# Optimization experiments

Measured on AMD Instinct MI355X. Metric: run time of the kernel, lower is better.

The kernel has to match this reference:

```python
import jax, jax.numpy as jnp
from jax import lax
import numpy as np

SIGMAS = (30.0, 150.0, 300.0)
RESTORE_FACTOR = 2.0
COLOR_GAIN = 10.0
GAIN = 270.0
OFFSET = 128.0
EPS = 1e-6


def _dwconv(x, k2d, stride):
    # depthwise 2D conv, NCHW, VALID padding (caller pads)
    C = x.shape[1]
    kh, kw = k2d.shape
    w = jnp.broadcast_to(k2d.astype(x.dtype)[None, None], (C, 1, kh, kw))
    return lax.conv_general_dilated(
        x, w, (stride, stride), 'VALID',
        dimension_numbers=('NCHW', 'OIHW', 'NCHW'),
        feature_group_count=C)


def _pyr_down(x):
    # cv2.pyrDown: 5x5 binomial kernel, reflect-101 border, stride-2 decimation
    k1 = jnp.array([1., 4., 6., 4., 1.], jnp.float32) / 16.0
    k2 = jnp.outer(k1, k1)
    xp = jnp.pad(x, ((0, 0), (0, 0), (2, 2), (2, 2)), mode='reflect')
    return _dwconv(xp, k2, 2)


def _gauss_blur(x, ksize):
    # cv2.GaussianBlur with sigmaX=0: sigma derived from kernel size
    s = 0.3 * ((ksize - 1) * 0.5 - 1.0) + 0.8
    i = jnp.arange(ksize, dtype=jnp.float32) - (ksize - 1) / 2.0
    g = jnp.exp(-(i * i) / (2.0 * s * s))
    g = g / g.sum()
    k2 = jnp.outer(g, g)
    p = ksize // 2
    xp = jnp.pad(x, ((0, 0), (0, 0), (p, p), (p, p)), mode='reflect')
    return _dwconv(xp, k2, 1)


def _fast_filter(x, sigma):
    # Faithful port of GaussianBlurConv.FastFilter (static Python recursion:
    # sigma is a compile-time constant, so depth is fixed at trace time).
    sigma = min(sigma, 300.0)
    k = int(round(sigma * 3 * 2 + 1)) | 1
    if k < 3:
        return x
    if k < 10:
        return _gauss_blur(x, k)
    h, w = x.shape[2], x.shape[3]
    if h < 2 or w < 2:
        return x
    sub = _fast_filter(_pyr_down(x), sigma / 2.0)
    # cv2.resize default INTER_LINEAR == half-pixel bilinear
    return jax.image.resize(sub, (x.shape[0], x.shape[1], h, w), method='bilinear')


def _msr_forward(x):
    img = x * 255.0 + 1.0                      # (N,3,H,W)
    log_img = jnp.log10(img + EPS)
    retinex = sum(log_img - jnp.log10(_fast_filter(img, s) + EPS) for s in SIGMAS)
    retinex = retinex / len(SIGMAS)
    img_sum = jnp.sum(img, axis=1, keepdims=True)   # (N,1,H,W)
    color_rest = jnp.log10(img * RESTORE_FACTOR / (img_sum + EPS) + 1.0)
    enhanced = retinex * color_rest * COLOR_GAIN * GAIN + OFFSET
    return jnp.clip(enhanced, 0.0, 255.0) / 255.0


def setup_inputs() -> dict:
    key = jax.random.key(0)
    x = jax.random.uniform(key, (8, 3, 1280, 1280), dtype=jnp.float32)
    return {"x": x}


def reference(x):
    return _msr_forward(x)
```

## Files before the change

kernel.cpp:

```cpp
#include <hip/hip_runtime.h>

#define NC 24

typedef float f32x4 __attribute__((ext_vector_type(4)));

__device__ __forceinline__ float pyr_point(const float* ip, int Hi, int Wi, int oy, int ox)
{
    const float k1[5] = {0.0625f, 0.25f, 0.375f, 0.25f, 0.0625f};
    float acc = 0.f;
#pragma unroll
    for (int i = 0; i < 5; ++i) {
        int y = 2 * oy - 2 + i;
        y = (y < 0) ? -y : y;
        y = (y >= Hi) ? (2 * Hi - 2 - y) : y;
        const float* rp = ip + (size_t)y * Wi;
        float r = 0.f;
#pragma unroll
        for (int j = 0; j < 5; ++j) {
            int xx = 2 * ox - 2 + j;
            xx = (xx < 0) ? -xx : xx;
            xx = (xx >= Wi) ? (2 * Wi - 2 - xx) : xx;
            r = fmaf(k1[j], rp[xx], r);
        }
        acc = fmaf(k1[i], r, acc);
    }
    return acc;
}

template <int K>
__device__ __forceinline__ float blur_point(const float* ip, int H, int W, int oy, int ox,
                                            const float* w)
{
    const int R = K / 2;
    float acc = 0.f;
#pragma unroll
    for (int i = 0; i < K; ++i) {
        int y = oy - R + i;
        y = (y < 0) ? -y : y;
        y = (y >= H) ? (2 * H - 2 - y) : y;
        const float* rp = ip + (size_t)y * W;
        float r = 0.f;
#pragma unroll
        for (int j = 0; j < K; ++j) {
            int xx = ox - R + j;
            xx = (xx < 0) ? -xx : xx;
            xx = (xx >= W) ? (2 * W - 2 - xx) : xx;
            r = fmaf(w[j], rp[xx], r);
        }
        acc = fmaf(w[i], r, acc);
    }
    return acc;
}

__global__ void __launch_bounds__(256) pyrdown4_kernel(
    const float* __restrict__ in, float* __restrict__ out,
    int Hi, int Wi, int Ho, int Wo, float scale, float offs)
{
    int qx = blockIdx.x * blockDim.x + threadIdx.x;
    int oy = blockIdx.y * blockDim.y + threadIdx.y;
    int nc = blockIdx.z;
    int ox0 = qx * 4;
    if (ox0 >= Wo || oy >= Ho) return;
    const float* ip = in + (size_t)nc * Hi * Wi;
    const float k[5] = {0.0625f, 0.25f, 0.375f, 0.25f, 0.0625f};

    bool fastx = (qx >= 1) && (8 * qx + 11 <= Wi - 1) && (ox0 + 3 < Wo);
    bool fasty = (oy >= 1) && (2 * oy + 2 <= Hi - 1);
    if (fastx && fasty) {
        int x0 = 8 * qx - 4;
        float col[11];
#pragma unroll
        for (int j = 0; j < 11; ++j) col[j] = 0.f;
        const float* rp = ip + (size_t)(2 * oy - 2) * Wi + x0;
#pragma unroll
        for (int i = 0; i < 5; ++i) {
            f32x4 a = *(const f32x4*)(rp);
            f32x4 b = *(const f32x4*)(rp + 4);
            f32x4 c4 = *(const f32x4*)(rp + 8);
            f32x4 d = *(const f32x4*)(rp + 12);
            float rv[16] = {a[0], a[1], a[2], a[3], b[0], b[1], b[2], b[3],
                            c4[0], c4[1], c4[2], c4[3], d[0], d[1], d[2], d[3]};
#pragma unroll
            for (int j = 0; j < 11; ++j) col[j] = fmaf(k[i], rv[j + 2], col[j]);
            rp += Wi;
        }
        f32x4 o;
#pragma unroll
        for (int p = 0; p < 4; ++p) {
            float s = 0.f;
#pragma unroll
            for (int j = 0; j < 5; ++j) s = fmaf(k[j], col[2 * p + j], s);
            o[p] = fmaf(s, scale, offs);
        }
        *(f32x4*)&out[((size_t)nc * Ho + oy) * Wo + ox0] = o;
    } else {
#pragma unroll
        for (int p = 0; p < 4; ++p) {
            int ox = ox0 + p;
            if (ox < Wo)
                out[((size_t)nc * Ho + oy) * Wo + ox] =
                    fmaf(pyr_point(ip, Hi, Wi, oy, ox), scale, offs);
        }
    }
}

__global__ void __launch_bounds__(256) base_kernel(
    const float* __restrict__ L4g, float* __restrict__ b30g,
    float* __restrict__ b150g, float* __restrict__ b300g)
{
    __shared__ float sL4[80 * 80];
    __shared__ float sL5[40 * 40];
    __shared__ float sL6[20 * 20];
    __shared__ float sL7[10 * 10];
    __shared__ float sL8[5 * 5];
    const int nc = blockIdx.x;
    const int tid = threadIdx.x;

    float w7[7], w9[9];
    {
        float s = 1.4f, s2 = 2.f * s * s, sum = 0.f;
#pragma unroll
        for (int i = 0; i < 7; ++i) { float d = (float)i - 3.f; w7[i] = expf(-(d * d) / s2); sum += w7[i]; }
#pragma unroll
        for (int i = 0; i < 7; ++i) w7[i] /= sum;
        s = 1.7f; s2 = 2.f * s * s; sum = 0.f;
#pragma unroll
        for (int i = 0; i < 9; ++i) { float d = (float)i - 4.f; w9[i] = expf(-(d * d) / s2); sum += w9[i]; }
#pragma unroll
        for (int i = 0; i < 9; ++i) w9[i] /= sum;
    }

    const float* src = L4g + (size_t)nc * 6400;
    for (int i = tid; i < 1600; i += 256)
        *(f32x4*)&sL4[4 * i] = *(const f32x4*)&src[4 * i];
    __syncthreads();
    for (int i = tid; i < 1600; i += 256) {
        int oy = i / 40, ox = i - oy * 40;
        sL5[i] = pyr_point(sL4, 80, 80, oy, ox);
    }
    __syncthreads();
    for (int i = tid; i < 400; i += 256) {
        int oy = i / 20, ox = i - oy * 20;
        sL6[i] = pyr_point(sL5, 40, 40, oy, ox);
    }
    __syncthreads();
    for (int i = tid; i < 100; i += 256) {
        int oy = i / 10, ox = i - oy * 10;
        sL7[i] = pyr_point(sL6, 20, 20, oy, ox);
    }
    __syncthreads();
    for (int i = tid; i < 25; i += 256) {
        int oy = i / 5, ox = i - oy * 5;
        sL8[i] = pyr_point(sL7, 10, 10, oy, ox);
    }
    __syncthreads();
    for (int i = tid; i < 1600; i += 256) {
        int oy = i / 40, ox = i - oy * 40;
        b30g[(size_t)nc * 1600 + i] = blur_point<7>(sL5, 40, 40, oy, ox, w7);
    }
    for (int i = tid; i < 100; i += 256) {
        int oy = i / 10, ox = i - oy * 10;
        b150g[(size_t)nc * 100 + i] = blur_point<9>(sL7, 10, 10, oy, ox, w9);
    }
    for (int i = tid; i < 25; i += 256) {
        int oy = i / 5, ox = i - oy * 5;
        b300g[(size_t)nc * 25 + i] = blur_point<9>(sL8, 5, 5, oy, ox, w9);
    }
}

__global__ void __launch_bounds__(256) mega_final(
    const float* __restrict__ x,
    const float* __restrict__ b30g,
    const float* __restrict__ b150g,
    const float* __restrict__ b300g,
    float* __restrict__ out)
{
    const int H = 1280, W = 1280;
    __shared__ float S[3 * 1963];

    const int tid = threadIdx.x;
    const int X0 = blockIdx.x * 64, Y0 = blockIdx.y * 64;
    const int n = blockIdx.z;

    const int LS[7] = {320, 160, 80, 40, 20, 10, 5};
    int ay[7], by[7], ax[7], bx[7];
    ay[0] = max(0, Y0 / 4 - 1); by[0] = min(319, Y0 / 4 + 16);
    ax[0] = max(0, X0 / 4 - 1); bx[0] = min(319, X0 / 4 + 16);
#pragma unroll
    for (int l = 1; l < 7; ++l) {
        ay[l] = max(0, (ay[l - 1] >> 1) - 1); by[l] = min(LS[l] - 1, (by[l - 1] >> 1) + 1);
        ax[l] = max(0, (ax[l - 1] >> 1) - 1); bx[l] = min(LS[l] - 1, (bx[l - 1] >> 1) + 1);
    }
    const int o300t[7] = {1639, 1495, 1414, 1365, 1329, 1293, 1268};
    const int o150t[6] = {944, 800, 719, 670, 634, 598};
    const int o30t[4]  = {274, 130, 49, 0};

    {
        int ny = by[3] - ay[3] + 1, nx = bx[3] - ax[3] + 1;
        for (int i = tid; i < 3 * ny * nx; i += 256) {
            int c = i / (ny * nx), pt = i - c * (ny * nx);
            int ry = pt / nx, rx = pt - ry * nx;
            S[c * 1963 + o30t[3] + pt] =
                b30g[(size_t)(n * 3 + c) * 1600 + (ay[3] + ry) * 40 + ax[3] + rx];
        }
        ny = by[5] - ay[5] + 1; nx = bx[5] - ax[5] + 1;
        for (int i = tid; i < 3 * ny * nx; i += 256) {
            int c = i / (ny * nx), pt = i - c * (ny * nx);
            int ry = pt / nx, rx = pt - ry * nx;
            S[c * 1963 + o150t[5] + pt] =
                b150g[(size_t)(n * 3 + c) * 100 + (ay[5] + ry) * 10 + ax[5] + rx];
        }
        ny = by[6] - ay[6] + 1; nx = bx[6] - ax[6] + 1;
        for (int i = tid; i < 3 * ny * nx; i += 256) {
            int c = i / (ny * nx), pt = i - c * (ny * nx);
            int ry = pt / nx, rx = pt - ry * nx;
            S[c * 1963 + o300t[6] + pt] =
                b300g[(size_t)(n * 3 + c) * 25 + (ay[6] + ry) * 5 + ax[6] + rx];
        }
    }
    __syncthreads();

#pragma unroll
    for (int l = 5; l >= 0; --l) {
        int srcO[9], dstO[9];
        int m = 0;
#pragma unroll
        for (int c = 0; c < 3; ++c) { srcO[m] = c * 1963 + o300t[l + 1]; dstO[m] = c * 1963 + o300t[l]; ++m; }
        if (l <= 4) {
#pragma unroll
            for (int c = 0; c < 3; ++c) { srcO[m] = c * 1963 + o150t[l + 1]; dstO[m] = c * 1963 + o150t[l]; ++m; }
        }
        if (l <= 2) {
#pragma unroll
            for (int c = 0; c < 3; ++c) { srcO[m] = c * 1963 + o30t[l + 1]; dstO[m] = c * 1963 + o30t[l]; ++m; }
        }
        int ny = by[l] - ay[l] + 1, nx = bx[l] - ax[l] + 1;
        int nxS = bx[l + 1] - ax[l + 1] + 1;
        int Ssrc = LS[l + 1];
        int npts = ny * nx;
        for (int i = tid; i < m * npts; i += 256) {
            int p = i / npts, pt = i - p * npts;
            int ry = pt / nx, rx = pt - ry * nx;
            int oy = ay[l] + ry, ox = ax[l] + rx;
            int my = oy >> 1, py = oy & 1;
            int mx = ox >> 1, px = ox & 1;
            int yA = py ? my : max(my - 1, 0);
            int yB = py ? min(my + 1, Ssrc - 1) : my;
            float wyA = py ? 0.75f : 0.25f, wyB = py ? 0.25f : 0.75f;
            int xA = px ? mx : max(mx - 1, 0);
            int xB = px ? min(mx + 1, Ssrc - 1) : mx;
            float wxA = px ? 0.75f : 0.25f, wxB = px ? 0.25f : 0.75f;
            const float* sp = &S[srcO[p]];
            int la = (yA - ay[l + 1]) * nxS - ax[l + 1];
            int lb = (yB - ay[l + 1]) * nxS - ax[l + 1];
            float v = wyA * (wxA * sp[la + xA] + wxB * sp[la + xB]) +
                      wyB * (wxA * sp[lb + xA] + wxB * sp[lb + xB]);
            S[dstO[p] + pt] = v;
        }
        __syncthreads();
    }

    int tyi = tid >> 4, txi = tid & 15;
    int byi = Y0 / 4 + tyi, bxi = X0 / 4 + txi;
    int nx0 = bx[0] - ax[0] + 1;
    int ry[3], rx[3];
    ry[0] = (byi > 0 ? byi - 1 : 0) - ay[0]; ry[1] = byi - ay[0];
    ry[2] = (byi < 319 ? byi + 1 : 319) - ay[0];
    rx[0] = (bxi > 0 ? bxi - 1 : 0) - ax[0]; rx[1] = bxi - ax[0];
    rx[2] = (bxi < 319 ? bxi + 1 : 319) - ax[0];
    const float WP[4][3] = {{0.375f, 0.625f, 0.f},
                            {0.1875f, 0.75f, 0.0625f},
                            {0.0625f, 0.75f, 0.1875f},
                            {0.f, 0.625f, 0.375f}};
    const int ol0[3] = {274, 944, 1639};

    f32x4 xi[3][4];
#pragma unroll
    for (int c = 0; c < 3; ++c)
#pragma unroll
        for (int qy = 0; qy < 4; ++qy)
            xi[c][qy] = __builtin_nontemporal_load(
                (const f32x4*)&x[((size_t)(n * 3 + c) * H + 4 * byi + qy) * W + 4 * bxi]);

    float crcp[4][4];
#pragma unroll
    for (int qy = 0; qy < 4; ++qy)
#pragma unroll
        for (int qx = 0; qx < 4; ++qx) {
            float s = (xi[0][qy][qx] + xi[1][qy][qx] + xi[2][qy][qx]) * 255.f + 3.f;
            crcp[qy][qx] = __fdividef(2.f, s + 1e-6f);
        }

#pragma unroll
    for (int c = 0; c < 3; ++c) {
        float prod[4][4];
#pragma unroll
        for (int qy = 0; qy < 4; ++qy)
#pragma unroll
            for (int qx = 0; qx < 4; ++qx) prod[qy][qx] = 1.f;

#pragma unroll
        for (int s = 0; s < 3; ++s) {
            const float* fp = &S[c * 1963 + ol0[s]];
            float v[3][3];
#pragma unroll
            for (int i = 0; i < 3; ++i)
#pragma unroll
                for (int j = 0; j < 3; ++j) v[i][j] = fp[ry[i] * nx0 + rx[j]];
#pragma unroll
            for (int qy = 0; qy < 4; ++qy) {
                float vy0 = WP[qy][0] * v[0][0] + WP[qy][1] * v[1][0] + WP[qy][2] * v[2][0];
                float vy1 = WP[qy][0] * v[0][1] + WP[qy][1] * v[1][1] + WP[qy][2] * v[2][1];
                float vy2 = WP[qy][0] * v[0][2] + WP[qy][1] * v[1][2] + WP[qy][2] * v[2][2];
#pragma unroll
                for (int qx = 0; qx < 4; ++qx) {
                    float val = WP[qx][0] * vy0 + WP[qx][1] * vy1 + WP[qx][2] * vy2;
                    prod[qy][qx] *= (val + 1e-6f);
                }
            }
        }

#pragma unroll
        for (int qy = 0; qy < 4; ++qy) {
            f32x4 o;
#pragma unroll
            for (int qx = 0; qx < 4; ++qx) {
                float img = xi[c][qy][qx] * 255.f + 1.f;
                float a = img + 1e-6f;
                float l2a = __log2f(__fdividef(a * a * a, prod[qy][qx]));
                float carg = fmaf(img, crcp[qy][qx], 1.f);
                float l2c = __log2f(carg);
                float e = fmaf(l2a * l2c, 81.55715246f, 128.f);
                e = fminf(fmaxf(e, 0.f), 255.f);
                o[qx] = e * (1.f / 255.f);
            }
            __builtin_nontemporal_store(
                o, (f32x4*)&out[((size_t)(n * 3 + c) * H + 4 * byi + qy) * W + 4 * bxi]);
        }
    }
}

extern "C" void kernel_launch(void* const* d_in, const int* in_sizes, int n_in,
                              void* d_out, int out_size, void* d_ws, size_t ws_size,
                              hipStream_t stream)
{
    const float* x = (const float*)d_in[0];
    float* out = (float*)d_out;
    float* ws = (float*)d_ws;

    size_t off = 0;
    auto alloc = [&](int d) { float* p = ws + off; off += (size_t)NC * d * d; return p; };
    float* L1 = alloc(640);
    float* L2 = alloc(320);
    float* L3 = alloc(160);
    float* L4 = alloc(80);
    float* b30 = alloc(40);
    float* b150 = alloc(10);
    float* b300 = alloc(5);
    (void)ws_size; (void)in_sizes; (void)n_in; (void)out_size;

    dim3 blk(32, 8, 1);
    auto grid4 = [&](int Wo, int Ho) { return dim3((Wo / 4 + 31) / 32, (Ho + 7) / 8, NC); };

    pyrdown4_kernel<<<grid4(640, 640), blk, 0, stream>>>(x,  L1, 1280, 1280, 640, 640, 255.f, 1.f);
    pyrdown4_kernel<<<grid4(320, 320), blk, 0, stream>>>(L1, L2, 640, 640, 320, 320, 1.f, 0.f);
    pyrdown4_kernel<<<grid4(160, 160), blk, 0, stream>>>(L2, L3, 320, 320, 160, 160, 1.f, 0.f);
    pyrdown4_kernel<<<grid4(80,  80),  blk, 0, stream>>>(L3, L4, 160, 160, 80, 80, 1.f, 0.f);
    base_kernel<<<dim3(NC, 1, 1), dim3(256, 1, 1), 0, stream>>>(L4, b30, b150, b300);
    mega_final<<<dim3(20, 20, 8), dim3(256, 1, 1), 0, stream>>>(x, b30, b150, b300, out);
}
```

Measured before the change: 424.7 us.

## Rewrite pyrDown as separable two-pass LDS-tiled kernel; factor bilinear upsample

```diff
diff --git a/kernel.cpp b/kernel.cpp
--- a/kernel.cpp
+++ b/kernel.cpp
@@ -52,55 +52,49 @@
     return acc;
 }
 
-__global__ void __launch_bounds__(256) pyrdown4_kernel(
+__global__ void __launch_bounds__(256) pyrdown_lds_kernel(
     const float* __restrict__ in, float* __restrict__ out,
     int Hi, int Wi, int Ho, int Wo, float scale, float offs)
 {
-    int qx = blockIdx.x * blockDim.x + threadIdx.x;
-    int oy = blockIdx.y * blockDim.y + threadIdx.y;
-    int nc = blockIdx.z;
-    int ox0 = qx * 4;
-    if (ox0 >= Wo || oy >= Ho) return;
+    const int TW = 132;
+    __shared__ float vs[16 * TW];
+    const int tid = threadIdx.x;
+    const int OX = blockIdx.x * 64;
+    const int OY = blockIdx.y * 16;
+    const int nc = blockIdx.z;
+    const float k1[5] = {0.0625f, 0.25f, 0.375f, 0.25f, 0.0625f};
     const float* ip = in + (size_t)nc * Hi * Wi;
-    const float k[5] = {0.0625f, 0.25f, 0.375f, 0.25f, 0.0625f};
-
-    bool fastx = (qx >= 1) && (8 * qx + 11 <= Wi - 1) && (ox0 + 3 < Wo);
-    bool fasty = (oy >= 1) && (2 * oy + 2 <= Hi - 1);
-    if (fastx && fasty) {
-        int x0 = 8 * qx - 4;
-        float col[11];
-#pragma unroll
-        for (int j = 0; j < 11; ++j) col[j] = 0.f;
-        const float* rp = ip + (size_t)(2 * oy - 2) * Wi + x0;
+
+    for (int idx = tid; idx < 16 * TW; idx += 256) {
+        int r = idx / TW;
+        int c = idx - r * TW;
+        int oy = OY + r;
+        if (oy >= Ho) oy = Ho - 1;
+        int xc = 2 * OX - 2 + c;
+        xc = (xc < 0) ? -xc : xc;
+        xc = (xc >= Wi) ? (2 * Wi - 2 - xc) : xc;
+        xc = max(0, min(Wi - 1, xc));
+        float acc = 0.f;
 #pragma unroll
         for (int i = 0; i < 5; ++i) {
-            f32x4 a = *(const f32x4*)(rp);
-            f32x4 b = *(const f32x4*)(rp + 4);
-            f32x4 c4 = *(const f32x4*)(rp + 8);
-            f32x4 d = *(const f32x4*)(rp + 12);
-            float rv[16] = {a[0], a[1], a[2], a[3], b[0], b[1], b[2], b[3],
-                            c4[0], c4[1], c4[2], c4[3], d[0], d[1], d[2], d[3]};
-#pragma unroll
-            for (int j = 0; j < 11; ++j) col[j] = fmaf(k[i], rv[j + 2], col[j]);
-            rp += Wi;
-        }
-        f32x4 o;
-#pragma unroll
-        for (int p = 0; p < 4; ++p) {
-            float s = 0.f;
-#pragma unroll
-            for (int j = 0; j < 5; ++j) s = fmaf(k[j], col[2 * p + j], s);
-            o[p] = fmaf(s, scale, offs);
-        }
-        *(f32x4*)&out[((size_t)nc * Ho + oy) * Wo + ox0] = o;
-    } else {
-#pragma unroll
-        for (int p = 0; p < 4; ++p) {
-            int ox = ox0 + p;
-            if (ox < Wo)
-                out[((size_t)nc * Ho + oy) * Wo + ox] =
-                    fmaf(pyr_point(ip, Hi, Wi, oy, ox), scale, offs);
-        }
+            int y = 2 * oy - 2 + i;
+            y = (y < 0) ? -y : y;
+            y = (y >= Hi) ? (2 * Hi - 2 - y) : y;
+            acc = fmaf(k1[i], ip[(size_t)y * Wi + xc], acc);
+        }
+        vs[idx] = acc;
+    }
+    __syncthreads();
+
+    for (int o = tid; o < 1024; o += 256) {
+        int r = o >> 6, c = o & 63;
+        int ox = OX + c, oy = OY + r;
+        if (ox >= Wo || oy >= Ho) continue;
+        const float* vp = &vs[r * TW + 2 * c];
+        float s = 0.f;
+#pragma unroll
+        for (int j = 0; j < 5; ++j) s = fmaf(k1[j], vp[j], s);
+        out[((size_t)nc * Ho + oy) * Wo + ox] = fmaf(s, scale, offs);
     }
 }
 
@@ -268,10 +262,6 @@
     ry[2] = (byi < 319 ? byi + 1 : 319) - ay[0];
     rx[0] = (bxi > 0 ? bxi - 1 : 0) - ax[0]; rx[1] = bxi - ax[0];
     rx[2] = (bxi < 319 ? bxi + 1 : 319) - ax[0];
-    const float WP[4][3] = {{0.375f, 0.625f, 0.f},
-                            {0.1875f, 0.75f, 0.0625f},
-                            {0.0625f, 0.75f, 0.1875f},
-                            {0.f, 0.625f, 0.375f}};
     const int ol0[3] = {274, 944, 1639};
 
     f32x4 xi[3][4];
@@ -307,16 +297,26 @@
             for (int i = 0; i < 3; ++i)
 #pragma unroll
                 for (int j = 0; j < 3; ++j) v[i][j] = fp[ry[i] * nx0 + rx[j]];
+            float cy[4][3];
+#pragma unroll
+            for (int j = 0; j < 3; ++j) {
+                float v0 = v[0][j], v1 = v[1][j], v2 = v[2][j];
+                cy[0][j] = fmaf(0.375f, v0, 0.625f * v1);
+                cy[1][j] = fmaf(0.1875f, v0, fmaf(0.75f, v1, 0.0625f * v2));
+                cy[2][j] = fmaf(0.0625f, v0, fmaf(0.75f, v1, 0.1875f * v2));
+                cy[3][j] = fmaf(0.625f, v1, 0.375f * v2);
+            }
 #pragma unroll
             for (int qy = 0; qy < 4; ++qy) {
-                float vy0 = WP[qy][0] * v[0][0] + WP[qy][1] * v[1][0] + WP[qy][2] * v[2][0];
-                float vy1 = WP[qy][0] * v[0][1] + WP[qy][1] * v[1][1] + WP[qy][2] * v[2][1];
-                float vy2 = WP[qy][0] * v[0][2] + WP[qy][1] * v[1][2] + WP[qy][2] * v[2][2];
-#pragma unroll
-                for (int qx = 0; qx < 4; ++qx) {
-                    float val = WP[qx][0] * vy0 + WP[qx][1] * vy1 + WP[qx][2] * vy2;
-                    prod[qy][qx] *= (val + 1e-6f);
-                }
+                float a0 = cy[qy][0], a1 = cy[qy][1], a2 = cy[qy][2];
+                float t0 = fmaf(0.375f, a0, 0.625f * a1);
+                float t1 = fmaf(0.1875f, a0, fmaf(0.75f, a1, 0.0625f * a2));
+                float t2 = fmaf(0.0625f, a0, fmaf(0.75f, a1, 0.1875f * a2));
+                float t3 = fmaf(0.625f, a1, 0.375f * a2);
+                prod[qy][0] *= (t0 + 1e-6f);
+                prod[qy][1] *= (t1 + 1e-6f);
+                prod[qy][2] *= (t2 + 1e-6f);
+                prod[qy][3] *= (t3 + 1e-6f);
             }
         }
 
@@ -359,13 +359,13 @@
     float* b300 = alloc(5);
     (void)ws_size; (void)in_sizes; (void)n_in; (void)out_size;
 
-    dim3 blk(32, 8, 1);
-    auto grid4 = [&](int Wo, int Ho) { return dim3((Wo / 4 + 31) / 32, (Ho + 7) / 8, NC); };
-
-    pyrdown4_kernel<<<grid4(640, 640), blk, 0, stream>>>(x,  L1, 1280, 1280, 640, 640, 255.f, 1.f);
-    pyrdown4_kernel<<<grid4(320, 320), blk, 0, stream>>>(L1, L2, 640, 640, 320, 320, 1.f, 0.f);
-    pyrdown4_kernel<<<grid4(160, 160), blk, 0, stream>>>(L2, L3, 320, 320, 160, 160, 1.f, 0.f);
-    pyrdown4_kernel<<<grid4(80,  80),  blk, 0, stream>>>(L3, L4, 160, 160, 80, 80, 1.f, 0.f);
+    dim3 blk(256, 1, 1);
+    auto gridP = [&](int Wo, int Ho) { return dim3((Wo + 63) / 64, (Ho + 15) / 16, NC); };
+
+    pyrdown_lds_kernel<<<gridP(640, 640), blk, 0, stream>>>(x,  L1, 1280, 1280, 640, 640, 255.f, 1.f);
+    pyrdown_lds_kernel<<<gridP(320, 320), blk, 0, stream>>>(L1, L2, 640, 640, 320, 320, 1.f, 0.f);
+    pyrdown_lds_kernel<<<gridP(160, 160), blk, 0, stream>>>(L2, L3, 320, 320, 160, 160, 1.f, 0.f);
+    pyrdown_lds_kernel<<<gridP(80,  80),  blk, 0, stream>>>(L3, L4, 160, 160, 80, 80, 1.f, 0.f);
     base_kernel<<<dim3(NC, 1, 1), dim3(256, 1, 1), 0, stream>>>(L4, b30, b150, b300);
     mega_final<<<dim3(20, 20, 8), dim3(256, 1, 1), 0, stream>>>(x, b30, b150, b300, out);
 }
```

Result: faster. 390.0 us (-8.2%).
